# Kernel optimization log

Hardware: AMD Instinct MI355X
Metric: run time of the kernel (lower is better)

## Reference

```python
import jax, jax.numpy as jnp
import numpy as np

LN_EPS = 1e-5

def setup_inputs() -> dict:
    key = jax.random.key(0)
    k1, k2, k3, k4 = jax.random.split(key, 4)
    B, N, F, O = 8, 2048, 256, 256
    x = jax.random.normal(k1, (B, N, F), dtype=jnp.float32)
    adj = jax.random.uniform(k2, (B, N, N), dtype=jnp.float32)
    # LayerNorm affine params
    gamma = jnp.ones((F,), jnp.float32)
    beta = jnp.zeros((F,), jnp.float32)
    # Linear weights stored as [in, out] (torch stores [out, in]; math identical)
    W_self = jax.random.normal(k3, (F, O), dtype=jnp.float32) * (1.0 / np.sqrt(F))
    W_neigh = jax.random.normal(k4, (F, O), dtype=jnp.float32) * (1.0 / np.sqrt(F))
    return {"x": x, "adj": adj, "gamma": gamma, "beta": beta,
            "W_self": W_self, "W_neigh": W_neigh}

def reference(x, adj, gamma, beta, W_self, W_neigh):
    # LayerNorm over last dim
    mu = jnp.mean(x, axis=-1, keepdims=True)
    var = jnp.mean(jnp.square(x - mu), axis=-1, keepdims=True)
    xn = (x - mu) * jax.lax.rsqrt(var + LN_EPS) * gamma + beta

    # Normalized Laplacian: I - D_out^{-1/2} A D_in^{-1/2}
    # out_degree = column sums (dim=1), in_degree = row sums (dim=2)
    d_out = jnp.sum(adj, axis=1)   # [B, N]
    d_in = jnp.sum(adj, axis=2)    # [B, N]
    s_out = jnp.where(d_out != 0, jax.lax.rsqrt(d_out), 0.0)
    s_in = jnp.where(d_in != 0, jax.lax.rsqrt(d_in), 0.0)
    # diag(s_out) @ A @ diag(s_in) == row/col elementwise rescale (no N^3 work)
    A_norm = s_out[:, :, None] * adj * s_in[:, None, :]
    eye = jnp.eye(adj.shape[1], dtype=adj.dtype)
    L = eye[None, :, :] - A_norm    # [B, N, N]

    neighbor = jnp.einsum('bij,bjf->bif', L, xn)   # [B, N, F]
    pre = xn @ W_self + neighbor @ W_neigh          # [B, N, O]
    return jax.nn.softplus(pre)
```

## Files before the change

kernel.cpp:

```cpp
#include <hip/hip_runtime.h>
#include <stdint.h>

#define B_ 8
#define N_ 2048
#define F_ 256

typedef unsigned short u16;
typedef __attribute__((ext_vector_type(8))) short bf16x8;
typedef __attribute__((ext_vector_type(4))) float f32x4;

__device__ __forceinline__ u16 f2bf(float f) {
    uint32_t u = __builtin_bit_cast(uint32_t, f);
    u += 0x7FFFu + ((u >> 16) & 1u);
    return (u16)(u >> 16);
}
__device__ __forceinline__ uint32_t pack2(float a, float b) {
    return (uint32_t)f2bf(a) | ((uint32_t)f2bf(b) << 16);
}

__device__ __forceinline__ void gload_lds16(const void* g, void* lds_uniform_base) {
    __builtin_amdgcn_global_load_lds(
        (const __attribute__((address_space(1))) uint32_t*)g,
        (__attribute__((address_space(3))) uint32_t*)lds_uniform_base, 16, 0, 0);
}

__global__ __launch_bounds__(256) void k_pre(const float* __restrict__ adj,
                                             const float* __restrict__ x,
                                             const float* __restrict__ gamma,
                                             const float* __restrict__ beta,
                                             u16* __restrict__ adj_bf,
                                             float* __restrict__ pcol,
                                             u16* __restrict__ xn,
                                             u16* __restrict__ yT) {
    const int b = blockIdx.y, panel = blockIdx.x;
    const int t = threadIdx.x, w = t >> 6, l = t & 63;
    __shared__ float rs[32][4];
    __shared__ u16 yt[256 * 34];
    const float* base = adj + ((size_t)b * N_ + (size_t)panel * 32) * N_;
    u16* abf = adj_bf + ((size_t)b * N_ + (size_t)panel * 32) * N_;
    float c0[4], c1[4];
#pragma unroll
    for (int e = 0; e < 4; ++e) { c0[e] = 0.f; c1[e] = 0.f; }
#pragma unroll 4
    for (int r = 0; r < 32; ++r) {
        const float4 v0 = *(const float4*)(base + (size_t)r * N_ + t * 4);
        const float4 v1 = *(const float4*)(base + (size_t)r * N_ + 1024 + t * 4);
        c0[0] += v0.x; c0[1] += v0.y; c0[2] += v0.z; c0[3] += v0.w;
        c1[0] += v1.x; c1[1] += v1.y; c1[2] += v1.z; c1[3] += v1.w;
        *(uint2*)&abf[(size_t)r * N_ + t * 4] = make_uint2(pack2(v0.x, v0.y), pack2(v0.z, v0.w));
        *(uint2*)&abf[(size_t)r * N_ + 1024 + t * 4] = make_uint2(pack2(v1.x, v1.y), pack2(v1.z, v1.w));
        float s = (v0.x + v0.y) + (v0.z + v0.w) + (v1.x + v1.y) + (v1.z + v1.w);
#pragma unroll
        for (int off = 32; off; off >>= 1) s += __shfl_xor(s, off);
        if (l == 0) rs[r][w] = s;
    }
    float4* pc = (float4*)(pcol + ((size_t)(b * 64 + panel)) * N_);
    pc[t]       = make_float4(c0[0], c0[1], c0[2], c0[3]);
    pc[t + 256] = make_float4(c1[0], c1[1], c1[2], c1[3]);
    __syncthreads();
    float g[4], be[4];
#pragma unroll
    for (int m = 0; m < 4; ++m) { g[m] = gamma[l + 64 * m]; be[m] = beta[l + 64 * m]; }
    for (int rr = 0; rr < 8; ++rr) {
        const int jj = w * 8 + rr;
        const int j = panel * 32 + jj;
        const float rowsum = rs[jj][0] + rs[jj][1] + rs[jj][2] + rs[jj][3];
        const float sin_ = (rowsum != 0.f) ? rsqrtf(rowsum) : 0.f;
        const float* xp = x + ((size_t)b * N_ + j) * F_;
        float v[4], s = 0.f, ss = 0.f;
#pragma unroll
        for (int m = 0; m < 4; ++m) { v[m] = xp[l + 64 * m]; s += v[m]; ss += v[m] * v[m]; }
#pragma unroll
        for (int off = 32; off; off >>= 1) { s += __shfl_xor(s, off); ss += __shfl_xor(ss, off); }
        const float mu = s * (1.f / 256.f);
        const float var = ss * (1.f / 256.f) - mu * mu;
        const float rstd = rsqrtf(var + 1e-5f);
        u16* xnp = xn + ((size_t)b * N_ + j) * F_;
#pragma unroll
        for (int m = 0; m < 4; ++m) {
            const float xv = (v[m] - mu) * rstd * g[m] + be[m];
            xnp[l + 64 * m] = f2bf(xv);
            yt[(l + 64 * m) * 34 + jj] = f2bf(sin_ * xv);
        }
    }
    __syncthreads();
#pragma unroll
    for (int m2 = 0; m2 < 2; ++m2) {
        const int f = (t >> 1) + 128 * m2;
        const int jj0 = (t & 1) * 16;
        uint32_t vals[8];
#pragma unroll
        for (int e = 0; e < 8; ++e) vals[e] = *(const uint32_t*)&yt[f * 34 + jj0 + 2 * e];
        uint4* dst = (uint4*)(yT + ((size_t)b * F_ + f) * N_ + panel * 32 + jj0);
        dst[0] = make_uint4(vals[0], vals[1], vals[2], vals[3]);
        dst[1] = make_uint4(vals[4], vals[5], vals[6], vals[7]);
    }
}

__global__ __launch_bounds__(256) void k_mid(const float* __restrict__ pcol,
                                             const float* __restrict__ Ws,
                                             const float* __restrict__ Wn,
                                             float* __restrict__ deg_col,
                                             u16* __restrict__ WcT,
                                             u16* __restrict__ WnT) {
    const int bx = blockIdx.x, t = threadIdx.x;
    if (bx < 64) {
        const int tid = bx * 256 + t;
        const int b = tid >> 11, j = tid & 2047;
        const float* p = pcol + (size_t)b * 64 * N_ + j;
        float s = 0.f;
#pragma unroll
        for (int g = 0; g < 64; ++g) s += p[(size_t)g * N_];
        deg_col[tid] = s;
    } else {
        const int rel = bx - 64;
#pragma unroll 4
        for (int e = 0; e < 32; ++e) {
            const int idx = rel * 8192 + e * 256 + t;
            const int k = idx >> 8, o = idx & 255;
            const float a = Ws[idx], q = Wn[idx];
            WcT[o * 256 + k] = f2bf(a + q);
            WnT[o * 256 + k] = f2bf(-q);
        }
    }
}

__global__ __launch_bounds__(256) void k_gemm1(const u16* __restrict__ adj_bf,
                                               const u16* __restrict__ yT,
                                               const float* __restrict__ deg_col,
                                               u16* __restrict__ z) {
    const int blk = blockIdx.x;
    const int b = blk & 7;
    const int kk = blk >> 3;
    const int nt = kk & 1;
    const int m = kk >> 1;
    const int i0 = m * 64, f0 = nt * 128;
    const int t = threadIdx.x, w = t >> 6, l = t & 63;
    const int wr = w >> 1, wc = w & 1;
    alignas(16) __shared__ u16 As[64 * 32];
    alignas(16) __shared__ u16 Bs[128 * 32];
    f32x4 acc[2][4];
#pragma unroll
    for (int mi = 0; mi < 2; ++mi)
#pragma unroll
        for (int ni = 0; ni < 4; ++ni) acc[mi][ni] = (f32x4)0.f;

    const u16* abase = adj_bf + ((size_t)b * N_ + i0) * N_;
    const u16* ybase = yT + ((size_t)b * F_ + f0) * (size_t)N_;
    const int lr = l >> 2, lb = (l & 3) * 16;

    for (int kt = 0; kt < 64; ++kt) {
        const int k0b = kt * 64;
        gload_lds16((const char*)(abase + (size_t)(w * 16 + lr) * N_) + k0b + lb,
                    (char*)As + (w << 10));
#pragma unroll
        for (int q = 0; q < 2; ++q)
            gload_lds16((const char*)(ybase + (size_t)(q * 64 + w * 16 + lr) * N_) + k0b + lb,
                        (char*)Bs + q * 4096 + (w << 10));
        __syncthreads();
        bf16x8 af[2], bfr[4];
#pragma unroll
        for (int mi = 0; mi < 2; ++mi)
            af[mi] = *(const bf16x8*)&As[(wr * 32 + mi * 16 + (l & 15)) * 32 + (l >> 4) * 8];
#pragma unroll
        for (int ni = 0; ni < 4; ++ni)
            bfr[ni] = *(const bf16x8*)&Bs[(wc * 64 + ni * 16 + (l & 15)) * 32 + (l >> 4) * 8];
#pragma unroll
        for (int mi = 0; mi < 2; ++mi)
#pragma unroll
            for (int ni = 0; ni < 4; ++ni)
                acc[mi][ni] = __builtin_amdgcn_mfma_f32_16x16x32_bf16(af[mi], bfr[ni], acc[mi][ni], 0, 0, 0);
        __syncthreads();
    }
#pragma unroll
    for (int mi = 0; mi < 2; ++mi) {
#pragma unroll
        for (int r = 0; r < 4; ++r) {
            const int row = i0 + wr * 32 + mi * 16 + (l >> 4) * 4 + r;
            const float d = deg_col[(size_t)b * N_ + row];
            const float so = (d != 0.f) ? rsqrtf(d) : 0.f;
#pragma unroll
            for (int ni = 0; ni < 4; ++ni) {
                const int col = f0 + wc * 64 + ni * 16 + (l & 15);
                z[((size_t)b * N_ + row) * F_ + col] = f2bf(so * acc[mi][ni][r]);
            }
        }
    }
}

__global__ __launch_bounds__(256) void k_gemm2(const u16* __restrict__ xn,
                                               const u16* __restrict__ z,
                                               const u16* __restrict__ WcT,
                                               const u16* __restrict__ WnT,
                                               float* __restrict__ out) {
    const int blk = blockIdx.x;
    const int xcd = blk & 7;
    const int kk = blk >> 3;
    const int nt = kk & 1;
    const int mt = xcd + 8 * (kk >> 1);
    const int r0 = mt * 64, o0 = nt * 128;
    const int t = threadIdx.x, w = t >> 6, l = t & 63;
    const int wr = w >> 1, wc = w & 1;
    alignas(16) __shared__ u16 As[64 * 32];
    alignas(16) __shared__ u16 Bs[128 * 32];
    f32x4 acc[2][4];
#pragma unroll
    for (int mi = 0; mi < 2; ++mi)
#pragma unroll
        for (int ni = 0; ni < 4; ++ni) acc[mi][ni] = (f32x4)0.f;

    const int lr = l >> 2, lb = (l & 3) * 16;

    for (int kt = 0; kt < 16; ++kt) {
        const u16* asrc = (kt < 8) ? xn : z;
        const u16* bsrc = (kt < 8) ? WcT : WnT;
        const int kk0b = (kt & 7) * 64;
        gload_lds16((const char*)(asrc + (size_t)(r0 + w * 16 + lr) * F_) + kk0b + lb,
                    (char*)As + (w << 10));
#pragma unroll
        for (int q = 0; q < 2; ++q)
            gload_lds16((const char*)(bsrc + (size_t)(o0 + q * 64 + w * 16 + lr) * F_) + kk0b + lb,
                        (char*)Bs + q * 4096 + (w << 10));
        __syncthreads();
        bf16x8 af[2], bfr[4];
#pragma unroll
        for (int mi = 0; mi < 2; ++mi)
            af[mi] = *(const bf16x8*)&As[(wr * 32 + mi * 16 + (l & 15)) * 32 + (l >> 4) * 8];
#pragma unroll
        for (int ni = 0; ni < 4; ++ni)
            bfr[ni] = *(const bf16x8*)&Bs[(wc * 64 + ni * 16 + (l & 15)) * 32 + (l >> 4) * 8];
#pragma unroll
        for (int mi = 0; mi < 2; ++mi)
#pragma unroll
            for (int ni = 0; ni < 4; ++ni)
                acc[mi][ni] = __builtin_amdgcn_mfma_f32_16x16x32_bf16(af[mi], bfr[ni], acc[mi][ni], 0, 0, 0);
        __syncthreads();
    }
#pragma unroll
    for (int mi = 0; mi < 2; ++mi) {
#pragma unroll
        for (int r = 0; r < 4; ++r) {
            const int rr = r0 + wr * 32 + mi * 16 + (l >> 4) * 4 + r;
#pragma unroll
            for (int ni = 0; ni < 4; ++ni) {
                const int cc = o0 + wc * 64 + ni * 16 + (l & 15);
                const float p = acc[mi][ni][r];
                out[(size_t)rr * F_ + cc] = (p > 20.f) ? p : log1pf(expf(p));
            }
        }
    }
}

extern "C" void kernel_launch(void* const* d_in, const int* in_sizes, int n_in,
                              void* d_out, int out_size, void* d_ws, size_t ws_size,
                              hipStream_t stream) {
    (void)in_sizes; (void)n_in; (void)out_size; (void)ws_size;
    const float* x     = (const float*)d_in[0];
    const float* adj   = (const float*)d_in[1];
    const float* gamma = (const float*)d_in[2];
    const float* beta  = (const float*)d_in[3];
    const float* Ws    = (const float*)d_in[4];
    const float* Wn    = (const float*)d_in[5];
    float* out = (float*)d_out;

    char* ws = (char*)d_ws;
    float* deg_col = (float*)(ws + 0);
    u16* xn     = (u16*)(ws + 65536);
    u16* yT     = (u16*)(ws + 8454144);
    u16* z      = (u16*)(ws + 16842752);
    u16* WcT    = (u16*)(ws + 25231360);
    u16* WnT    = (u16*)(ws + 25362432);
    u16* adj_bf = (u16*)(ws + 25493504);
    float* pcol = (float*)z;

    k_pre  <<<dim3(64, 8), 256, 0, stream>>>(adj, x, gamma, beta, adj_bf, pcol, xn, yT);
    k_mid  <<<72, 256, 0, stream>>>(pcol, Ws, Wn, deg_col, WcT, WnT);
    k_gemm1<<<512, 256, 0, stream>>>(adj_bf, yT, deg_col, z);
    k_gemm2<<<512, 256, 0, stream>>>(xn, z, WcT, WnT, out);
}
```

Measured before the change: 303.7 us.

## Split adjacency pass into finer-grained kernel and move LayerNorm into mid kernel

The adjacency conversion and degree pass now runs on 2048 blocks, each covering 16 rows and half a row width, instead of 512 blocks of 32 full rows. Row-sum partials go to a new buffer, and the LayerNorm/transpose work moves into the mid kernel alongside the column-degree and weight preparation. The goal is more parallelism and better bandwidth use in the memory-bound adjacency stream. In exchange, the partial column sums buffer doubles in size and the degree reduction has more terms to add.

```diff
diff --git a/kernel.cpp b/kernel.cpp
--- a/kernel.cpp
+++ b/kernel.cpp
@@ -24,96 +24,101 @@
         (__attribute__((address_space(3))) uint32_t*)lds_uniform_base, 16, 0, 0);
 }
 
-__global__ __launch_bounds__(256) void k_pre(const float* __restrict__ adj,
-                                             const float* __restrict__ x,
+__global__ __launch_bounds__(256) void k_adj(const float* __restrict__ adj,
+                                             u16* __restrict__ adj_bf,
+                                             float* __restrict__ pcol,
+                                             float* __restrict__ prow) {
+    const int panel = blockIdx.x, half = blockIdx.y, b = blockIdx.z;
+    const int t = threadIdx.x, w = t >> 6, l = t & 63;
+    const float* base = adj + ((size_t)b * N_ + (size_t)panel * 16) * N_ + half * 1024;
+    u16* abf = adj_bf + ((size_t)b * N_ + (size_t)panel * 16) * N_ + half * 1024;
+    float c[4];
+#pragma unroll
+    for (int e = 0; e < 4; ++e) c[e] = 0.f;
+    __shared__ float rs[16][4];
+#pragma unroll 4
+    for (int r = 0; r < 16; ++r) {
+        const float4 v = *(const float4*)(base + (size_t)r * N_ + t * 4);
+        c[0] += v.x; c[1] += v.y; c[2] += v.z; c[3] += v.w;
+        *(uint2*)&abf[(size_t)r * N_ + t * 4] = make_uint2(pack2(v.x, v.y), pack2(v.z, v.w));
+        float s = (v.x + v.y) + (v.z + v.w);
+#pragma unroll
+        for (int off = 32; off; off >>= 1) s += __shfl_xor(s, off);
+        if (l == 0) rs[r][w] = s;
+    }
+    float4* pc = (float4*)(pcol + ((size_t)(b * 128 + panel)) * N_ + half * 1024);
+    pc[t] = make_float4(c[0], c[1], c[2], c[3]);
+    __syncthreads();
+    if (t < 16)
+        prow[(size_t)half * (B_ * N_) + (size_t)b * N_ + panel * 16 + t]
+            = rs[t][0] + rs[t][1] + rs[t][2] + rs[t][3];
+}
+
+__global__ __launch_bounds__(256) void k_mid(const float* __restrict__ x,
                                              const float* __restrict__ gamma,
                                              const float* __restrict__ beta,
-                                             u16* __restrict__ adj_bf,
-                                             float* __restrict__ pcol,
-                                             u16* __restrict__ xn,
-                                             u16* __restrict__ yT) {
-    const int b = blockIdx.y, panel = blockIdx.x;
-    const int t = threadIdx.x, w = t >> 6, l = t & 63;
-    __shared__ float rs[32][4];
-    __shared__ u16 yt[256 * 34];
-    const float* base = adj + ((size_t)b * N_ + (size_t)panel * 32) * N_;
-    u16* abf = adj_bf + ((size_t)b * N_ + (size_t)panel * 32) * N_;
-    float c0[4], c1[4];
-#pragma unroll
-    for (int e = 0; e < 4; ++e) { c0[e] = 0.f; c1[e] = 0.f; }
-#pragma unroll 4
-    for (int r = 0; r < 32; ++r) {
-        const float4 v0 = *(const float4*)(base + (size_t)r * N_ + t * 4);
-        const float4 v1 = *(const float4*)(base + (size_t)r * N_ + 1024 + t * 4);
-        c0[0] += v0.x; c0[1] += v0.y; c0[2] += v0.z; c0[3] += v0.w;
-        c1[0] += v1.x; c1[1] += v1.y; c1[2] += v1.z; c1[3] += v1.w;
-        *(uint2*)&abf[(size_t)r * N_ + t * 4] = make_uint2(pack2(v0.x, v0.y), pack2(v0.z, v0.w));
-        *(uint2*)&abf[(size_t)r * N_ + 1024 + t * 4] = make_uint2(pack2(v1.x, v1.y), pack2(v1.z, v1.w));
-        float s = (v0.x + v0.y) + (v0.z + v0.w) + (v1.x + v1.y) + (v1.z + v1.w);
-#pragma unroll
-        for (int off = 32; off; off >>= 1) s += __shfl_xor(s, off);
-        if (l == 0) rs[r][w] = s;
-    }
-    float4* pc = (float4*)(pcol + ((size_t)(b * 64 + panel)) * N_);
-    pc[t]       = make_float4(c0[0], c0[1], c0[2], c0[3]);
-    pc[t + 256] = make_float4(c1[0], c1[1], c1[2], c1[3]);
-    __syncthreads();
-    float g[4], be[4];
-#pragma unroll
-    for (int m = 0; m < 4; ++m) { g[m] = gamma[l + 64 * m]; be[m] = beta[l + 64 * m]; }
-    for (int rr = 0; rr < 8; ++rr) {
-        const int jj = w * 8 + rr;
-        const int j = panel * 32 + jj;
-        const float rowsum = rs[jj][0] + rs[jj][1] + rs[jj][2] + rs[jj][3];
-        const float sin_ = (rowsum != 0.f) ? rsqrtf(rowsum) : 0.f;
-        const float* xp = x + ((size_t)b * N_ + j) * F_;
-        float v[4], s = 0.f, ss = 0.f;
-#pragma unroll
-        for (int m = 0; m < 4; ++m) { v[m] = xp[l + 64 * m]; s += v[m]; ss += v[m] * v[m]; }
-#pragma unroll
-        for (int off = 32; off; off >>= 1) { s += __shfl_xor(s, off); ss += __shfl_xor(ss, off); }
-        const float mu = s * (1.f / 256.f);
-        const float var = ss * (1.f / 256.f) - mu * mu;
-        const float rstd = rsqrtf(var + 1e-5f);
-        u16* xnp = xn + ((size_t)b * N_ + j) * F_;
-#pragma unroll
-        for (int m = 0; m < 4; ++m) {
-            const float xv = (v[m] - mu) * rstd * g[m] + be[m];
-            xnp[l + 64 * m] = f2bf(xv);
-            yt[(l + 64 * m) * 34 + jj] = f2bf(sin_ * xv);
-        }
-    }
-    __syncthreads();
-#pragma unroll
-    for (int m2 = 0; m2 < 2; ++m2) {
-        const int f = (t >> 1) + 128 * m2;
-        const int jj0 = (t & 1) * 16;
-        uint32_t vals[8];
-#pragma unroll
-        for (int e = 0; e < 8; ++e) vals[e] = *(const uint32_t*)&yt[f * 34 + jj0 + 2 * e];
-        uint4* dst = (uint4*)(yT + ((size_t)b * F_ + f) * N_ + panel * 32 + jj0);
-        dst[0] = make_uint4(vals[0], vals[1], vals[2], vals[3]);
-        dst[1] = make_uint4(vals[4], vals[5], vals[6], vals[7]);
-    }
-}
-
-__global__ __launch_bounds__(256) void k_mid(const float* __restrict__ pcol,
+                                             const float* __restrict__ prow,
+                                             const float* __restrict__ pcol,
                                              const float* __restrict__ Ws,
                                              const float* __restrict__ Wn,
+                                             u16* __restrict__ xn,
+                                             u16* __restrict__ yT,
                                              float* __restrict__ deg_col,
                                              u16* __restrict__ WcT,
                                              u16* __restrict__ WnT) {
-    const int bx = blockIdx.x, t = threadIdx.x;
-    if (bx < 64) {
-        const int tid = bx * 256 + t;
+    const int bx = blockIdx.x;
+    const int t = threadIdx.x;
+    __shared__ u16 yt[256 * 34];
+    if (bx < 512) {
+        const int b = bx >> 6, panel = bx & 63;
+        const int w = t >> 6, l = t & 63;
+        float g[4], be[4];
+#pragma unroll
+        for (int m = 0; m < 4; ++m) { g[m] = gamma[l + 64 * m]; be[m] = beta[l + 64 * m]; }
+        for (int rr = 0; rr < 8; ++rr) {
+            const int jj = w * 8 + rr;
+            const int j = panel * 32 + jj;
+            const float rowsum = prow[(size_t)b * N_ + j] + prow[(size_t)(B_ * N_) + (size_t)b * N_ + j];
+            const float sin_ = (rowsum != 0.f) ? rsqrtf(rowsum) : 0.f;
+            const float* xp = x + ((size_t)b * N_ + j) * F_;
+            float v[4], s = 0.f, ss = 0.f;
+#pragma unroll
+            for (int m = 0; m < 4; ++m) { v[m] = xp[l + 64 * m]; s += v[m]; ss += v[m] * v[m]; }
+#pragma unroll
+            for (int off = 32; off; off >>= 1) { s += __shfl_xor(s, off); ss += __shfl_xor(ss, off); }
+            const float mu = s * (1.f / 256.f);
+            const float var = ss * (1.f / 256.f) - mu * mu;
+            const float rstd = rsqrtf(var + 1e-5f);
+            u16* xnp = xn + ((size_t)b * N_ + j) * F_;
+#pragma unroll
+            for (int m = 0; m < 4; ++m) {
+                const float xv = (v[m] - mu) * rstd * g[m] + be[m];
+                xnp[l + 64 * m] = f2bf(xv);
+                yt[(l + 64 * m) * 34 + jj] = f2bf(sin_ * xv);
+            }
+        }
+        __syncthreads();
+#pragma unroll
+        for (int m2 = 0; m2 < 2; ++m2) {
+            const int f = (t >> 1) + 128 * m2;
+            const int jj0 = (t & 1) * 16;
+            uint32_t vals[8];
+#pragma unroll
+            for (int e = 0; e < 8; ++e) vals[e] = *(const uint32_t*)&yt[f * 34 + jj0 + 2 * e];
+            uint4* dst = (uint4*)(yT + ((size_t)b * F_ + f) * N_ + panel * 32 + jj0);
+            dst[0] = make_uint4(vals[0], vals[1], vals[2], vals[3]);
+            dst[1] = make_uint4(vals[4], vals[5], vals[6], vals[7]);
+        }
+    } else if (bx < 576) {
+        const int tid = (bx - 512) * 256 + t;
         const int b = tid >> 11, j = tid & 2047;
-        const float* p = pcol + (size_t)b * 64 * N_ + j;
+        const float* p = pcol + (size_t)b * 128 * N_ + j;
         float s = 0.f;
-#pragma unroll
-        for (int g = 0; g < 64; ++g) s += p[(size_t)g * N_];
+#pragma unroll 8
+        for (int g = 0; g < 128; ++g) s += p[(size_t)g * N_];
         deg_col[tid] = s;
     } else {
-        const int rel = bx - 64;
+        const int rel = bx - 576;
 #pragma unroll 4
         for (int e = 0; e < 32; ++e) {
             const int idx = rel * 8192 + e * 256 + t;
@@ -265,16 +270,18 @@
 
     char* ws = (char*)d_ws;
     float* deg_col = (float*)(ws + 0);
-    u16* xn     = (u16*)(ws + 65536);
-    u16* yT     = (u16*)(ws + 8454144);
-    u16* z      = (u16*)(ws + 16842752);
-    u16* WcT    = (u16*)(ws + 25231360);
-    u16* WnT    = (u16*)(ws + 25362432);
-    u16* adj_bf = (u16*)(ws + 25493504);
+    float* prow    = (float*)(ws + 65536);
+    u16* xn     = (u16*)(ws + 196608);
+    u16* yT     = (u16*)(ws + 8585216);
+    u16* z      = (u16*)(ws + 16973824);
+    u16* WcT    = (u16*)(ws + 25362432);
+    u16* WnT    = (u16*)(ws + 25493504);
+    u16* adj_bf = (u16*)(ws + 25624576);
     float* pcol = (float*)z;
 
-    k_pre  <<<dim3(64, 8), 256, 0, stream>>>(adj, x, gamma, beta, adj_bf, pcol, xn, yT);
-    k_mid  <<<72, 256, 0, stream>>>(pcol, Ws, Wn, deg_col, WcT, WnT);
+    k_adj  <<<dim3(128, 2, 8), 256, 0, stream>>>(adj, adj_bf, pcol, prow);
+    k_mid  <<<584, 256, 0, stream>>>(x, gamma, beta, prow, pcol, Ws, Wn,
+                                     xn, yT, deg_col, WcT, WnT);
     k_gemm1<<<512, 256, 0, stream>>>(adj_bf, yT, deg_col, z);
     k_gemm2<<<512, 256, 0, stream>>>(xn, z, WcT, WnT, out);
 }
```

Result: no change. 304.3 us (+0.2%).
